# Kernel optimization log

Hardware: AMD Instinct MI355X
Metric: run time of the kernel (lower is better)

Reference implementation:

```python
import jax, jax.numpy as jnp
import numpy as np
import math

N = 512; B = 32; T_IN = 24; T_OUT = 12; C_IN = 1; C_OUT = 64
D_MODEL = 64; N_HEADS = 8; K = 3; N_LAYERS = 2; D_FF = 4 * D_MODEL
MA_KERNEL = 25; FACTOR = 1
E_HEAD = D_MODEL // N_HEADS


def _sin_pe(T, d):
    pos = jnp.arange(T, dtype=jnp.float32)[:, None]
    div = jnp.exp(jnp.arange(0, d, 2, dtype=jnp.float32) * (-math.log(10000.0) / d))
    pe = jnp.zeros((T, d), dtype=jnp.float32)
    pe = pe.at[:, 0::2].set(jnp.sin(pos * div))
    pe = pe.at[:, 1::2].set(jnp.cos(pos * div))
    return pe


def _moving_avg(x, k):
    # Autoformer series_decomp moving average with edge-replicate padding. x: (B,L,D)
    pad = (k - 1) // 2
    xp = jnp.concatenate([jnp.repeat(x[:, :1], pad, axis=1), x, jnp.repeat(x[:, -1:], pad, axis=1)], axis=1)
    cs = jnp.cumsum(xp, axis=1)
    cs = jnp.concatenate([jnp.zeros_like(cs[:, :1]), cs], axis=1)
    return (cs[:, k:] - cs[:, :-k]) / k


def _autocorr_attn(q, k, v):
    # Autoformer AutoCorrelation (eval-mode delay aggregation). q,k,v: (Bf,L,H,E)
    Bf, L, H, E = q.shape
    qf = jnp.fft.rfft(jnp.transpose(q, (0, 2, 3, 1)), axis=-1)
    kf = jnp.fft.rfft(jnp.transpose(k, (0, 2, 3, 1)), axis=-1)
    corr = jnp.fft.irfft(qf * jnp.conj(kf), n=L, axis=-1)      # (Bf,H,E,L)
    values = jnp.transpose(v, (0, 2, 3, 1))                    # (Bf,H,E,L)
    top_k = int(FACTOR * math.log(L))
    mean_value = corr.mean(axis=(1, 2))                        # (Bf,L)
    weights, delay = jax.lax.top_k(mean_value, top_k)          # (Bf,top_k)
    tmp_corr = jax.nn.softmax(weights, axis=-1)
    base = jnp.arange(L)[None, :]
    agg = jnp.zeros_like(values)
    for i in range(top_k):
        idx = (base + delay[:, i:i + 1]) % L                   # circular gather == repeat+gather
        pattern = jnp.take_along_axis(values, idx[:, None, None, :], axis=-1)
        agg = agg + pattern * tmp_corr[:, i][:, None, None, None]
    return jnp.transpose(agg, (0, 3, 1, 2))                    # (Bf,L,H,E)


def _forward(s_w, x, swnn_w, swnn_b, alpha, beta, theta, wq, bq, wk, bk, wv, bv, wo, bo,
             conv1_w, conv1_b, conv2_w, conv2_b, norm_g, norm_b, dec_w, dec_b,
             slin_w, slin_b, tlin_w, tlin_b):
    W = jax.nn.softmax(s_w @ swnn_w.T + swnn_b, axis=1)        # SWNN, n_hidden=1
    Lmat = jnp.diag(W.sum(axis=1)) - W
    lam = jax.lax.stop_gradient(jnp.max(jnp.real(jnp.linalg.eigvals(Lmat))))
    Lt = 2.0 * Lmat / lam - jnp.eye(N, dtype=x.dtype)
    chebs = [jnp.eye(N, dtype=x.dtype), Lt]
    for i in range(2, K):
        chebs.append(2.0 * Lt * chebs[-1] - chebs[-2])         # elementwise *, as in the source
    w_x = jnp.einsum('btnc,nm->btmc', x, W)
    s_acc = jnp.zeros((B, T_IN, N, C_OUT), dtype=x.dtype)
    for kk in range(K):
        s_r = alpha[kk] + jnp.einsum('btnc,co->btno', x, beta[kk]) + jnp.einsum('btnc,co->btno', w_x, theta[kk])
        s_acc = s_acc + jnp.einsum('btno,nm->btmo', s_r, chebs[kk])
    s_out = jax.nn.relu(jnp.transpose(s_acc, (0, 2, 3, 1)))    # (B,N,O,T_in)
    s_out = jnp.einsum('bnot,ut->bnou', s_out, slin_w) + slin_b  # (B,N,O,T_out)
    # ---- temporal branch: PE + AutoCorrelation encoder (AutoTRGCN) ----
    x_bnct = jnp.transpose(x, (0, 2, 3, 1))                    # (B,N,C,T)
    h = x_bnct[..., None] + _sin_pe(T_IN, D_MODEL)             # (B,N,C,T,D)
    h = h.reshape(B * N * C_IN, T_IN, D_MODEL)
    for _ in range(N_LAYERS):                                  # shared layer params, as in source
        q = (jnp.einsum('bld,ed->ble', h, wq) + bq).reshape(-1, T_IN, N_HEADS, E_HEAD)
        kt = (jnp.einsum('bld,ed->ble', h, wk) + bk).reshape(-1, T_IN, N_HEADS, E_HEAD)
        vt = (jnp.einsum('bld,ed->ble', h, wv) + bv).reshape(-1, T_IN, N_HEADS, E_HEAD)
        new_h = _autocorr_attn(q, kt, vt).reshape(-1, T_IN, D_MODEL)
        new_h = jnp.einsum('bld,ed->ble', new_h, wo) + bo
        h = h + new_h
        h = h - _moving_avg(h, MA_KERNEL)                      # series_decomp residual
        y = jax.nn.relu(jnp.einsum('bld,fd->blf', h, conv1_w) + conv1_b)
        y = jnp.einsum('blf,df->bld', y, conv2_w) + conv2_b
        hy = h + y
        h = hy - _moving_avg(hy, MA_KERNEL)
    mu = h.mean(-1, keepdims=True)
    var = ((h - mu) ** 2).mean(-1, keepdims=True)
    hn = (h - mu) / jnp.sqrt(var + 1e-5) * norm_g + norm_b
    h = hn - hn.mean(axis=1, keepdims=True)                    # my_Layernorm
    h = h.reshape(B, N, C_IN, T_IN * D_MODEL)
    t_out = jax.nn.relu(jnp.einsum('bnck,uk->bncu', h, dec_w) + dec_b)  # (B,N,C,T_out)
    t_out = jnp.einsum('bnct,oc->bnot', t_out, tlin_w) + tlin_b[None, None, :, None]  # (B,N,O,T_out)
    st = jax.nn.relu(s_out * t_out)
    return jnp.transpose(st, (0, 3, 1, 2))                     # (B,T_out,N,O)


def setup_inputs() -> dict:
    key = jax.random.key(0)
    ks = jax.random.split(key, 32)
    def rn(i, shape, scale=0.05):
        return jax.random.normal(ks[i], shape, dtype=jnp.float32) * scale
    return dict(
        s_w=jax.random.uniform(ks[0], (N, N), dtype=jnp.float32),
        x=jax.random.normal(ks[1], (B, T_IN, N, C_IN), dtype=jnp.float32),
        swnn_w=rn(2, (N, N)), swnn_b=rn(3, (N,)),
        alpha=rn(4, (K,)), beta=rn(5, (K, C_IN, C_OUT)), theta=rn(6, (K, C_IN, C_OUT)),
        wq=rn(7, (D_MODEL, D_MODEL)), bq=rn(8, (D_MODEL,)),
        wk=rn(9, (D_MODEL, D_MODEL)), bk=rn(10, (D_MODEL,)),
        wv=rn(11, (D_MODEL, D_MODEL)), bv=rn(12, (D_MODEL,)),
        wo=rn(13, (D_MODEL, D_MODEL)), bo=rn(14, (D_MODEL,)),
        conv1_w=rn(15, (D_FF, D_MODEL)), conv1_b=rn(16, (D_FF,)),
        conv2_w=rn(17, (D_MODEL, D_FF)), conv2_b=rn(18, (D_MODEL,)),
        norm_g=jnp.ones((D_MODEL,), dtype=jnp.float32), norm_b=jnp.zeros((D_MODEL,), dtype=jnp.float32),
        dec_w=rn(19, (T_OUT, D_MODEL * T_IN)), dec_b=rn(20, (T_OUT,)),
        slin_w=rn(21, (T_OUT, T_IN)), slin_b=rn(22, (T_OUT,)),
        tlin_w=rn(23, (C_OUT, C_IN)), tlin_b=rn(24, (C_OUT,)),
    )


def reference(s_w, x, swnn_w, swnn_b, alpha, beta, theta, wq, bq, wk, bk, wv, bv, wo, bo,
              conv1_w, conv1_b, conv2_w, conv2_b, norm_g, norm_b, dec_w, dec_b,
              slin_w, slin_b, tlin_w, tlin_b):
    return _forward(s_w, x, swnn_w, swnn_b, alpha, beta, theta, wq, bq, wk, bk, wv, bv, wo, bo,
                    conv1_w, conv1_b, conv2_w, conv2_b, norm_g, norm_b, dec_w, dec_b,
                    slin_w, slin_b, tlin_w, tlin_b)
```

## Files before the change

### kernel.cpp

```cpp
#include <hip/hip_runtime.h>
#include <hip/hip_bf16.h>
#include <math.h>


static const size_t OFF_W   = 0;
static const size_t OFF_SA  = OFF_W  + 512*512;
static const size_t OFF_SB  = OFF_SA + 512*512;
static const size_t OFF_WX  = OFF_SB + 512*512;
static const size_t OFF_Y1  = OFF_WX + 768*512;
static const size_t OFF_Y2  = OFF_Y1 + 768*512;
static const size_t OFF_Z1  = OFF_Y2 + 768*512;
static const size_t OFF_Z2  = OFF_Z1 + 768*512;
static const size_t OFF_TR  = OFF_Z2 + 768*512;
static const size_t OFF_PE  = OFF_TR + 16384*12;
static const size_t OFF_CS1 = OFF_PE + 24*64;
static const size_t OFF_CS2 = OFF_CS1 + 512;
static const size_t OFF_V0  = OFF_CS2 + 512;
static const size_t OFF_V1  = OFF_V0 + 512;
static const size_t OFF_NA  = OFF_V1 + 512;
static const size_t OFF_SC  = OFF_NA + 64;
static const size_t OFF_M   = OFF_SC + 16;
static const size_t OFF_PT  = OFF_M  + 4096;
static const size_t OFF_C1T = OFF_PT + 4096;
static const size_t OFF_C2T = OFF_C1T + 16384;
static const size_t OFF_BVO = OFF_C2T + 16384;

#define EIG_H 0.125f
#define EIG_K 14
#define MV_STEPS 32

__global__ __launch_bounds__(256) void k_prep(float* __restrict__ wsf) {
  const int t = threadIdx.x;
  for (int idx = t; idx < 24 * 64; idx += 256) {
    int l = idx >> 6, d = idx & 63;
    int i = d >> 1;
    float div = expf((float)(2 * i) * (-9.210340371976184f / 64.0f));
    float ang = (float)l * div;
    wsf[OFF_PE + idx] = (d & 1) ? cosf(ang) : sinf(ang);
  }
  for (int idx = t; idx < 512; idx += 256)
    wsf[OFF_V0 + idx] = sinf((float)idx * 12.9898f + 0.5f) + 0.01f;
  for (int idx = t; idx < 64; idx += 256)
    wsf[OFF_NA + idx] = 0.0f;
}

__global__ __launch_bounds__(256) void k_wprep(
    const float* __restrict__ wq, const float* __restrict__ wk,
    const float* __restrict__ wv, const float* __restrict__ wo,
    const float* __restrict__ bv, const float* __restrict__ bo,
    const float* __restrict__ c1w, const float* __restrict__ c2w,
    float* __restrict__ wsf) {
  const int blk = blockIdx.x, t = threadIdx.x;
  if (blk == 0) {
    for (int i = 0; i < 16; ++i) {
      int idx = i * 256 + t;
      int d = idx >> 6, dp = idx & 63;
      float s = 0.f;
      for (int e = 0; e < 64; ++e) s += wq[e * 64 + d] * wk[e * 64 + dp];
      wsf[OFF_M + idx] = s;
    }
    if (t < 64) {
      float s = bo[t];
      for (int f = 0; f < 64; ++f) s += wo[t * 64 + f] * bv[f];
      wsf[OFF_BVO + t] = s;
    }
  } else if (blk == 1) {
    for (int i = 0; i < 16; ++i) {
      int idx = i * 256 + t;
      int d = idx >> 6, e = idx & 63;
      float s = 0.f;
      for (int f = 0; f < 64; ++f) s += wo[e * 64 + f] * wv[f * 64 + d];
      wsf[OFF_PT + idx] = s;
    }
  } else if (blk < 4) {
    int base = (blk - 2) * 8192;
    for (int i = 0; i < 32; ++i) {
      int idx = base + i * 256 + t;
      int d = idx >> 8, f = idx & 255;
      wsf[OFF_C1T + idx] = c1w[f * 64 + d];
    }
  } else {
    int base = (blk - 4) * 8192;
    for (int i = 0; i < 32; ++i) {
      int idx = base + i * 256 + t;
      int f = idx >> 6, e = idx & 63;
      wsf[OFF_C2T + idx] = c2w[e * 256 + f];
    }
  }
}

__global__ __launch_bounds__(256) void k_gemm_logits(
    const float* __restrict__ A, const float* __restrict__ Bm,
    const float* __restrict__ bias, float* __restrict__ C) {
  __shared__ float As[32][33], Bs[32][33];
  const int tx = threadIdx.x & 31, ty = threadIdx.x >> 5;
  const int rb = blockIdx.y * 32, cb = blockIdx.x * 32;
  float acc[4] = {0.f, 0.f, 0.f, 0.f};
  for (int kk = 0; kk < 512; kk += 32) {
    for (int idx = threadIdx.x; idx < 1024; idx += 256) {
      int r = idx >> 5, c = idx & 31;
      As[r][c] = A[(rb + r) * 512 + kk + c];
      Bs[c][r] = Bm[(cb + r) * 512 + kk + c];
    }
    __syncthreads();
    for (int k2 = 0; k2 < 32; ++k2) {
      float bvv = Bs[k2][tx];
      #pragma unroll
      for (int i = 0; i < 4; ++i) acc[i] += As[ty + 8 * i][k2] * bvv;
    }
    __syncthreads();
  }
  float bb = bias[cb + tx];
  #pragma unroll
  for (int i = 0; i < 4; ++i)
    C[(rb + ty + 8 * i) * 512 + cb + tx] = acc[i] + bb;
}

__global__ __launch_bounds__(64) void k_softmax_rows(float* __restrict__ W) {
  const int r = blockIdx.x, t = threadIdx.x;
  float* row = W + (size_t)r * 512;
  float v[8];
  float mx = -3.4e38f;
  #pragma unroll
  for (int i = 0; i < 8; ++i) { v[i] = row[t + 64 * i]; mx = fmaxf(mx, v[i]); }
  for (int m = 1; m < 64; m <<= 1) mx = fmaxf(mx, __shfl_xor(mx, m));
  float s = 0.f;
  #pragma unroll
  for (int i = 0; i < 8; ++i) { v[i] = expf(v[i] - mx); s += v[i]; }
  for (int m = 1; m < 64; m <<= 1) s += __shfl_xor(s, m);
  float inv = 1.0f / s;
  #pragma unroll
  for (int i = 0; i < 8; ++i) row[t + 64 * i] = v[i] * inv;
}

__global__ __launch_bounds__(256) void k_init_S(float* __restrict__ wsf) {
  const int idx = blockIdx.x * 256 + threadIdx.x;
  const int i = idx >> 9, j = idx & 511;
  float w = wsf[OFF_W + idx];
  wsf[OFF_SA + idx] = ((i == j) ? 1.0f : 0.0f) - EIG_H * w;
  if (idx == 0) {
    wsf[OFF_SC + 0] = 0.0f;
    wsf[OFF_SC + 1] = 1.0f;
    ((unsigned int*)(wsf + OFF_SC))[8] = 0u;
  }
}

__global__ __launch_bounds__(256) void k_gemm_square(
    const float* __restrict__ A, float* __restrict__ C,
    const float* __restrict__ scal, unsigned int* __restrict__ mbits) {
  __shared__ float As[32][33], Bs[32][33];
  const int tx = threadIdx.x & 31, ty = threadIdx.x >> 5;
  const int rb = blockIdx.y * 32, cb = blockIdx.x * 32;
  float acc[4] = {0.f, 0.f, 0.f, 0.f};
  for (int kk = 0; kk < 512; kk += 32) {
    for (int idx = threadIdx.x; idx < 1024; idx += 256) {
      int r = idx >> 5, c = idx & 31;
      As[r][c] = A[(rb + r) * 512 + kk + c];
      Bs[r][c] = A[(kk + r) * 512 + cb + c];
    }
    __syncthreads();
    for (int k2 = 0; k2 < 32; ++k2) {
      float bvv = Bs[k2][tx];
      #pragma unroll
      for (int i = 0; i < 4; ++i) acc[i] += As[ty + 8 * i][k2] * bvv;
    }
    __syncthreads();
  }
  const float s = scal[1];
  const float s2 = s * s;
  float lmax = 0.f;
  #pragma unroll
  for (int i = 0; i < 4; ++i) {
    float v = acc[i] * s2;
    C[(rb + ty + 8 * i) * 512 + cb + tx] = v;
    lmax = fmaxf(lmax, fabsf(v));
  }
  for (int m = 1; m < 64; m <<= 1) lmax = fmaxf(lmax, __shfl_xor(lmax, m));
  if ((threadIdx.x & 63) == 0) atomicMax(mbits, __float_as_uint(lmax));
}

__global__ void k_bookkeep(float* __restrict__ wsf) {
  unsigned int* mb = (unsigned int*)(wsf + OFF_SC) + 8;
  float m = fmaxf(__uint_as_float(*mb), 1e-30f);
  wsf[OFF_SC + 0] = 2.0f * wsf[OFF_SC + 0] + logf(m);
  wsf[OFF_SC + 1] = 1.0f / m;
  *mb = 0u;
}

__global__ __launch_bounds__(64) void k_matvec(
    const float* __restrict__ S, const float* __restrict__ vin,
    float* __restrict__ vout, float* __restrict__ wsf, int p) {
  __shared__ float vv[512];
  const int t = threadIdx.x;
  const float invm = wsf[OFF_SC + 1];
  const float pn = (p == 0) ? 1.0f : fmaxf(wsf[OFF_NA + p - 1], 1e-30f);
  const float sc = invm / sqrtf(pn);
  for (int i = t; i < 512; i += 64) vv[i] = vin[i];
  __syncthreads();
  const int row = blockIdx.x * 64 + t;
  const float* rp = S + (size_t)row * 512;
  float acc = 0.f;
  for (int j = 0; j < 512; j += 4) {
    float4 a = *(const float4*)(rp + j);
    acc += a.x * vv[j] + a.y * vv[j + 1] + a.z * vv[j + 2] + a.w * vv[j + 3];
  }
  float y = acc * sc;
  vout[row] = y;
  float ss = y * y;
  for (int m = 1; m < 64; m <<= 1) ss += __shfl_xor(ss, m);
  if (t == 0) atomicAdd(&wsf[OFF_NA + p], ss);
}

__global__ void k_lamfin(float* __restrict__ wsf) {
  float slope = 0.f;
  for (int p = 8; p < 32; ++p) slope += 0.5f * logf(fmaxf(wsf[OFF_NA + p], 1e-30f));
  slope *= (1.0f / 24.0f);
  float rate = (slope + wsf[OFF_SC + 0]) * (1.0f / 16384.0f);
  float minre = (1.0f - expf(rate)) * (1.0f / EIG_H);
  float lam = 1.0f - minre;
  wsf[OFF_SC + 2] = lam;
  wsf[OFF_SC + 3] = 2.0f / lam - 1.0f;
  wsf[OFF_SC + 4] = 2.0f / lam;
}

__global__ __launch_bounds__(64) void k_colsum(const float* __restrict__ W,
                                               float* __restrict__ wsf) {
  const int m = blockIdx.x * 64 + threadIdx.x;
  float s1 = 0.f, s2 = 0.f;
  for (int n = 0; n < 512; ++n) {
    float w = W[n * 512 + m];
    s1 += w; s2 += w * w;
  }
  float wmm = W[m * 512 + m];
  float a = wsf[OFF_SC + 3], c = wsf[OFF_SC + 4];
  wsf[OFF_CS1 + m] = a - c * s1;
  wsf[OFF_CS2 + m] = 2.0f * (c * c * s2 + a * a - 2.0f * a * c * wmm) - 1.0f;
}

__global__ __launch_bounds__(256) void k_gemm_wx(
    const float* __restrict__ A, const float* __restrict__ Bm,
    float* __restrict__ C) {
  __shared__ float As[32][33], Bs[32][33];
  const int tx = threadIdx.x & 31, ty = threadIdx.x >> 5;
  const int rb = blockIdx.y * 32, cb = blockIdx.x * 32;
  float acc[4] = {0.f, 0.f, 0.f, 0.f};
  for (int kk = 0; kk < 512; kk += 32) {
    for (int idx = threadIdx.x; idx < 1024; idx += 256) {
      int r = idx >> 5, c = idx & 31;
      As[r][c] = A[(rb + r) * 512 + kk + c];
      Bs[r][c] = Bm[(kk + r) * 512 + cb + c];
    }
    __syncthreads();
    for (int k2 = 0; k2 < 32; ++k2) {
      float bvv = Bs[k2][tx];
      #pragma unroll
      for (int i = 0; i < 4; ++i) acc[i] += As[ty + 8 * i][k2] * bvv;
    }
    __syncthreads();
  }
  #pragma unroll
  for (int i = 0; i < 4; ++i)
    C[(rb + ty + 8 * i) * 512 + cb + tx] = acc[i];
}

__global__ __launch_bounds__(256) void k_gemm_yz(
    const float* __restrict__ X, const float* __restrict__ WX,
    const float* __restrict__ W, const float* __restrict__ sc,
    float* __restrict__ y1, float* __restrict__ y2,
    float* __restrict__ z1, float* __restrict__ z2) {
  __shared__ float Xs[32][33], Ms[32][33], C1s[32][33], C2s[32][33];
  const int tx = threadIdx.x & 31, ty = threadIdx.x >> 5;
  const int rb = blockIdx.y * 32, cb = blockIdx.x * 32;
  const float a = sc[3], c = sc[4];
  float ay1[4] = {0,0,0,0}, ay2[4] = {0,0,0,0}, az1[4] = {0,0,0,0}, az2[4] = {0,0,0,0};
  for (int kk = 0; kk < 512; kk += 32) {
    for (int idx = threadIdx.x; idx < 1024; idx += 256) {
      int r = idx >> 5, cc = idx & 31;
      Xs[r][cc] = X[(rb + r) * 512 + kk + cc];
      Ms[r][cc] = WX[(rb + r) * 512 + kk + cc];
      float w = W[(kk + r) * 512 + cb + cc];
      float dl = ((kk + r) == (cb + cc)) ? 1.0f : 0.0f;
      float c1 = a * dl - c * w;
      C1s[r][cc] = c1;
      C2s[r][cc] = 2.0f * c1 * c1 - dl;
    }
    __syncthreads();
    for (int k2 = 0; k2 < 32; ++k2) {
      float b1 = C1s[k2][tx], b2 = C2s[k2][tx];
      #pragma unroll
      for (int i = 0; i < 4; ++i) {
        float xv = Xs[ty + 8 * i][k2];
        float wv = Ms[ty + 8 * i][k2];
        ay1[i] += xv * b1; ay2[i] += xv * b2;
        az1[i] += wv * b1; az2[i] += wv * b2;
      }
    }
    __syncthreads();
  }
  #pragma unroll
  for (int i = 0; i < 4; ++i) {
    int off = (rb + ty + 8 * i) * 512 + cb + tx;
    y1[off] = ay1[i]; y2[off] = ay2[i];
    z1[off] = az1[i]; z2[off] = az2[i];
  }
}

#define HSTR 66
#define HSTR2 33

__device__ __forceinline__ void decomp_cols(float* __restrict__ hl, int t) {
  #pragma unroll
  for (int task = 0; task < 2; ++task) {
    int id = task * 256 + t;
    int sq = id >> 6, e = id & 63;
    int base = sq * 24 * HSTR + e;
    float h24[24];
    #pragma unroll
    for (int ll = 0; ll < 24; ++ll) h24[ll] = hl[base + ll * HSTR];
    float W = 13.0f * h24[0];
    #pragma unroll
    for (int j = 1; j <= 12; ++j) W += h24[j];
    #pragma unroll
    for (int ll = 0; ll < 24; ++ll) {
      hl[base + ll * HSTR] = h24[ll] - W * (1.0f / 25.0f);
      int jp = (ll + 13 > 23) ? 23 : ll + 13;
      int jm = (ll - 12 < 0) ? 0 : ll - 12;
      W += h24[jp] - h24[jm];
    }
  }
}

__global__ __launch_bounds__(256, 3) void k_temporal3(
    const float* __restrict__ x, const float* __restrict__ pe,
    const float* __restrict__ Mw, const float* __restrict__ PTw,
    const float* __restrict__ C1T, const float* __restrict__ C2T,
    const float* __restrict__ bvo,
    const float* __restrict__ c1b, const float* __restrict__ c2b,
    const float* __restrict__ ng, const float* __restrict__ nbv,
    const float* __restrict__ decw, const float* __restrict__ decb,
    float* __restrict__ trelu) {
  __shared__ float hl[8 * 24 * HSTR];
  __shared__ float aux[512];
  float* corr_s = aux;
  float* wsm_s  = aux + 192;
  int*   dly_s  = (int*)(aux + 216);
  float* cmean_s = aux;
  float* pr_s   = aux;

  const int t = threadIdx.x;
  const int s0 = blockIdx.x * 8;
  const bool active = t < 192;
  const int r = t;
  const int seq = r / 24;
  const int l = r - seq * 24;
  const int gseq = s0 + seq;
  const int b = gseq >> 9, n = gseq & 511;
  float2* hl2 = (float2*)hl;
  const int row2 = r * HSTR2;

  if (active) {
    float xv = x[(b * 24 + l) * 512 + n];
    const float2* per = (const float2*)(pe + l * 64);
    #pragma unroll
    for (int c = 0; c < 32; ++c) {
      float2 pv = per[c];
      hl2[row2 + c] = make_float2(xv + pv.x, xv + pv.y);
    }
  }
  __syncthreads();

  for (int layer = 0; layer < 2; ++layer) {
    if (t < 192) corr_s[t] = 0.f;
    __syncthreads();
    if (active) {
      float u[64];
      #pragma unroll
      for (int e = 0; e < 64; ++e) u[e] = 0.f;
      for (int dd = 0; dd < 32; ++dd) {
        float2 hv = hl2[row2 + dd];
        const float* M0 = Mw + (2 * dd) * 64;
        const float* M1 = M0 + 64;
        #pragma unroll
        for (int e = 0; e < 64; ++e) u[e] += hv.x * M0[e] + hv.y * M1[e];
      }
      for (int tau = 0; tau < 24; ++tau) {
        int l2v = l - tau; if (l2v < 0) l2v += 24;
        int bb2 = (seq * 24 + l2v) * HSTR2;
        float acc = 0.f;
        #pragma unroll
        for (int dd = 0; dd < 32; ++dd) {
          float2 h2 = hl2[bb2 + dd];
          acc += u[2 * dd] * h2.x + u[2 * dd + 1] * h2.y;
        }
        atomicAdd(&corr_s[seq * 24 + tau], acc * (1.0f / 64.0f));
      }
    }
    __syncthreads();
    if (t < 8) {
      const float* cr = corr_s + t * 24;
      int i0 = 0, i1 = 0, i2 = 0;
      float v0 = -3.4e38f, v1 = -3.4e38f, v2 = -3.4e38f;
      for (int j = 0; j < 24; ++j) { float v = cr[j]; if (v > v0) { v0 = v; i0 = j; } }
      for (int j = 0; j < 24; ++j) { if (j == i0) continue; float v = cr[j]; if (v > v1) { v1 = v; i1 = j; } }
      for (int j = 0; j < 24; ++j) { if (j == i0 || j == i1) continue; float v = cr[j]; if (v > v2) { v2 = v; i2 = j; } }
      float e1 = expf(v1 - v0), e2 = expf(v2 - v0);
      float inv = 1.0f / (1.0f + e1 + e2);
      wsm_s[t * 3] = inv; wsm_s[t * 3 + 1] = e1 * inv; wsm_s[t * 3 + 2] = e2 * inv;
      dly_s[t * 3] = i0; dly_s[t * 3 + 1] = i1; dly_s[t * 3 + 2] = i2;
    }
    __syncthreads();
    {
      float acc[64];
      #pragma unroll
      for (int e = 0; e < 64; ++e) acc[e] = 0.f;
      if (active) {
        float w0 = wsm_s[seq * 3], w1 = wsm_s[seq * 3 + 1], w2 = wsm_s[seq * 3 + 2];
        int d0 = dly_s[seq * 3], d1 = dly_s[seq * 3 + 1], d2 = dly_s[seq * 3 + 2];
        int l0 = l + d0; if (l0 >= 24) l0 -= 24;
        int l1 = l + d1; if (l1 >= 24) l1 -= 24;
        int l2 = l + d2; if (l2 >= 24) l2 -= 24;
        int b0 = (seq * 24 + l0) * HSTR2, b1 = (seq * 24 + l1) * HSTR2, b2 = (seq * 24 + l2) * HSTR2;
        for (int dd = 0; dd < 32; ++dd) {
          float2 a0 = hl2[b0 + dd], a1 = hl2[b1 + dd], av2 = hl2[b2 + dd];
          float gx = w0 * a0.x + w1 * a1.x + w2 * av2.x;
          float gy = w0 * a0.y + w1 * a1.y + w2 * av2.y;
          const float* P0 = PTw + (2 * dd) * 64;
          const float* P1 = P0 + 64;
          #pragma unroll
          for (int e = 0; e < 64; ++e) acc[e] += gx * P0[e] + gy * P1[e];
        }
      }
      __syncthreads();
      if (active) {
        #pragma unroll
        for (int j = 0; j < 32; ++j) {
          float2 cur = hl2[row2 + j];
          cur.x += acc[2 * j] + bvo[2 * j];
          cur.y += acc[2 * j + 1] + bvo[2 * j + 1];
          hl2[row2 + j] = cur;
        }
      }
    }
    __syncthreads();
    decomp_cols(hl, t);
    __syncthreads();
    {
      float a2[64];
      #pragma unroll
      for (int e = 0; e < 64; ++e) a2[e] = 0.f;
      if (active) {
        for (int fc = 0; fc < 16; ++fc) {
          float y16[16];
          #pragma unroll
          for (int f = 0; f < 16; ++f) y16[f] = 0.f;
          for (int dd = 0; dd < 32; ++dd) {
            float2 hv = hl2[row2 + dd];
            const float* c1a = C1T + (2 * dd) * 256 + fc * 16;
            const float* c1bp = c1a + 256;
            #pragma unroll
            for (int f = 0; f < 16; ++f) y16[f] += hv.x * c1a[f] + hv.y * c1bp[f];
          }
          #pragma unroll
          for (int f = 0; f < 16; ++f)
            y16[f] = fmaxf(y16[f] + c1b[fc * 16 + f], 0.0f);
          #pragma unroll
          for (int f = 0; f < 16; ++f) {
            float yf = y16[f];
            const float* r2 = C2T + (fc * 16 + f) * 64;
            #pragma unroll
            for (int e = 0; e < 64; ++e) a2[e] += yf * r2[e];
          }
        }
        #pragma unroll
        for (int j = 0; j < 32; ++j) {
          float2 cur = hl2[row2 + j];
          cur.x += a2[2 * j] + c2b[2 * j];
          cur.y += a2[2 * j + 1] + c2b[2 * j + 1];
          hl2[row2 + j] = cur;
        }
      }
    }
    __syncthreads();
    decomp_cols(hl, t);
    __syncthreads();
  }

  if (active) {
    float mu = 0.f;
    #pragma unroll
    for (int dd = 0; dd < 32; ++dd) { float2 v = hl2[row2 + dd]; mu += v.x + v.y; }
    mu *= (1.0f / 64.0f);
    float vs = 0.f;
    #pragma unroll
    for (int dd = 0; dd < 32; ++dd) {
      float2 v = hl2[row2 + dd];
      float dx = v.x - mu, dy = v.y - mu;
      vs += dx * dx + dy * dy;
    }
    float rs = rsqrtf(vs * (1.0f / 64.0f) + 1e-5f);
    #pragma unroll
    for (int dd = 0; dd < 32; ++dd) {
      float2 v = hl2[row2 + dd];
      v.x = (v.x - mu) * rs * ng[2 * dd] + nbv[2 * dd];
      v.y = (v.y - mu) * rs * ng[2 * dd + 1] + nbv[2 * dd + 1];
      hl2[row2 + dd] = v;
    }
  }
  __syncthreads();
  #pragma unroll
  for (int pass = 0; pass < 2; ++pass) {
    int idx = pass * 256 + t;
    int sq2 = idx >> 6, e2 = idx & 63;
    float s = 0.f;
    for (int ll = 0; ll < 24; ++ll) s += hl[(sq2 * 24 + ll) * HSTR + e2];
    cmean_s[idx] = s * (1.0f / 24.0f);
  }
  __syncthreads();
  if (active) {
    #pragma unroll
    for (int j = 0; j < 32; ++j) {
      float2 v = hl2[row2 + j];
      v.x -= cmean_s[seq * 64 + 2 * j];
      v.y -= cmean_s[seq * 64 + 2 * j + 1];
      hl2[row2 + j] = v;
    }
  }
  __syncthreads();
  if (active) {
    int g = t >> 3;
    int u = g >> 1, half = g & 1;
    int sq = t & 7;
    const float2* dwp2 = (const float2*)(decw + u * 1536 + half * 768);
    int hb2 = (sq * 24 + half * 12) * HSTR2;
    float part = 0.f;
    for (int j = 0; j < 384; ++j) {
      int lr = j >> 5, dd = j & 31;
      float2 hv = hl2[hb2 + lr * HSTR2 + dd];
      float2 wv = dwp2[j];
      part += hv.x * wv.x + hv.y * wv.y;
    }
    pr_s[t] = part;
  }
  __syncthreads();
  if (t < 96) {
    int u = t >> 3, sq = t & 7;
    float v = pr_s[(u * 2) * 8 + sq] + pr_s[(u * 2 + 1) * 8 + sq] + decb[u];
    trelu[(size_t)(s0 + sq) * 12 + u] = fmaxf(v, 0.0f);
  }
}

__global__ __launch_bounds__(64) void k_final(
    const float* __restrict__ x, const float* __restrict__ wx,
    const float* __restrict__ y1, const float* __restrict__ y2,
    const float* __restrict__ z1, const float* __restrict__ z2,
    const float* __restrict__ cs1, const float* __restrict__ cs2,
    const float* __restrict__ trelu,
    const float* __restrict__ alpha, const float* __restrict__ beta,
    const float* __restrict__ theta,
    const float* __restrict__ slinw, const float* __restrict__ slinb,
    const float* __restrict__ tlinw, const float* __restrict__ tlinb,
    float* __restrict__ out) {
  __shared__ float ly0[24], ly1[24], ly2[24], lz0[24], lz1[24], lz2[24];
  __shared__ float ltr[12], lsw[288];
  const int blk = blockIdx.x;
  const int b = blk >> 9, m = blk & 511;
  const int t = threadIdx.x;
  if (t < 24) {
    int row = (b * 24 + t) * 512 + m;
    ly0[t] = x[row];  ly1[t] = y1[row]; ly2[t] = y2[row];
    lz0[t] = wx[row]; lz1[t] = z1[row]; lz2[t] = z2[row];
  }
  if (t >= 48 && t < 60) ltr[t - 48] = trelu[(b * 512 + m) * 12 + (t - 48)];
  for (int i = t; i < 288; i += 64) lsw[i] = slinw[i];
  __syncthreads();
  const int o = t;
  const float at = alpha[0] + alpha[1] * cs1[m] + alpha[2] * cs2[m];
  const float b0 = beta[o], b1 = beta[64 + o], b2 = beta[128 + o];
  const float t0 = theta[o], t1 = theta[64 + o], t2 = theta[128 + o];
  float so[12];
  #pragma unroll
  for (int u = 0; u < 12; ++u) so[u] = 0.f;
  for (int tt = 0; tt < 24; ++tt) {
    float v = at + b0 * ly0[tt] + b1 * ly1[tt] + b2 * ly2[tt]
                 + t0 * lz0[tt] + t1 * lz1[tt] + t2 * lz2[tt];
    v = fmaxf(v, 0.0f);
    #pragma unroll
    for (int u = 0; u < 12; ++u) so[u] += lsw[u * 24 + tt] * v;
  }
  const float tw = tlinw[o], tb = tlinb[o];
  #pragma unroll
  for (int u = 0; u < 12; ++u) {
    float sval = so[u] + slinb[u];
    float tval = tw * ltr[u] + tb;
    float rr = fmaxf(sval * tval, 0.0f);
    out[(((size_t)b * 12 + u) * 512 + m) * 64 + o] = rr;
  }
}

extern "C" void kernel_launch(void* const* d_in, const int* in_sizes, int n_in,
                              void* d_out, int out_size, void* d_ws, size_t ws_size,
                              hipStream_t stream) {
  (void)in_sizes; (void)n_in; (void)out_size; (void)ws_size;
  const float* s_w    = (const float*)d_in[0];
  const float* x      = (const float*)d_in[1];
  const float* swnn_w = (const float*)d_in[2];
  const float* swnn_b = (const float*)d_in[3];
  const float* alpha  = (const float*)d_in[4];
  const float* beta   = (const float*)d_in[5];
  const float* theta  = (const float*)d_in[6];
  const float* wq = (const float*)d_in[7];  const float* bq = (const float*)d_in[8];
  const float* wk = (const float*)d_in[9];  const float* bk = (const float*)d_in[10];
  const float* wv = (const float*)d_in[11]; const float* bv = (const float*)d_in[12];
  const float* wo = (const float*)d_in[13]; const float* bo = (const float*)d_in[14];
  const float* c1w = (const float*)d_in[15]; const float* c1b = (const float*)d_in[16];
  const float* c2w = (const float*)d_in[17]; const float* c2b = (const float*)d_in[18];
  const float* ng  = (const float*)d_in[19]; const float* nb  = (const float*)d_in[20];
  const float* decw = (const float*)d_in[21]; const float* decb = (const float*)d_in[22];
  const float* slinw = (const float*)d_in[23]; const float* slinb = (const float*)d_in[24];
  const float* tlinw = (const float*)d_in[25]; const float* tlinb = (const float*)d_in[26];
  (void)bq; (void)bk;

  float* wsf = (float*)d_ws;
  float* out = (float*)d_out;

  float* Wm = wsf + OFF_W;
  float* Sa = wsf + OFF_SA;
  float* Sb = wsf + OFF_SB;
  unsigned int* mbits = (unsigned int*)(wsf + OFF_SC) + 8;
  const float* scal = wsf + OFF_SC;

  k_prep<<<1, 256, 0, stream>>>(wsf);
  k_wprep<<<6, 256, 0, stream>>>(wq, wk, wv, wo, bv, bo, c1w, c2w, wsf);
  k_gemm_logits<<<dim3(16, 16), 256, 0, stream>>>(s_w, swnn_w, swnn_b, Wm);
  k_softmax_rows<<<512, 64, 0, stream>>>(Wm);

  k_temporal3<<<2048, 256, 0, stream>>>(x, wsf + OFF_PE, wsf + OFF_M, wsf + OFF_PT,
                                        wsf + OFF_C1T, wsf + OFF_C2T, wsf + OFF_BVO,
                                        c1b, c2b, ng, nb, decw, decb, wsf + OFF_TR);

  k_init_S<<<1024, 256, 0, stream>>>(wsf);
  float* cur = Sa;
  float* nxt = Sb;
  for (int j = 0; j < EIG_K; ++j) {
    k_gemm_square<<<dim3(16, 16), 256, 0, stream>>>(cur, nxt, scal, mbits);
    k_bookkeep<<<1, 1, 0, stream>>>(wsf);
    float* tmp = cur; cur = nxt; nxt = tmp;
  }
  float* va = wsf + OFF_V0;
  float* vb = wsf + OFF_V1;
  for (int p = 0; p < MV_STEPS; ++p) {
    k_matvec<<<8, 64, 0, stream>>>(cur, va, vb, wsf, p);
    float* tmp = va; va = vb; vb = tmp;
  }
  k_lamfin<<<1, 1, 0, stream>>>(wsf);

  k_colsum<<<8, 64, 0, stream>>>(Wm, wsf);
  k_gemm_wx<<<dim3(16, 24), 256, 0, stream>>>(x, Wm, wsf + OFF_WX);
  k_gemm_yz<<<dim3(16, 24), 256, 0, stream>>>(x, wsf + OFF_WX, Wm, scal,
                                              wsf + OFF_Y1, wsf + OFF_Y2,
                                              wsf + OFF_Z1, wsf + OFF_Z2);
  k_final<<<16384, 64, 0, stream>>>(x, wsf + OFF_WX, wsf + OFF_Y1, wsf + OFF_Y2,
                                    wsf + OFF_Z1, wsf + OFF_Z2,
                                    wsf + OFF_CS1, wsf + OFF_CS2, wsf + OFF_TR,
                                    alpha, beta, theta, slinw, slinb,
                                    tlinw, tlinb, out);
}
```

Baseline: 2.888 ms.

## Enlarge square-GEMM tiles, halve power-iteration steps, vectorise temporal loads

The repeated-squaring GEMM moves from 32x32 tiles with 4 outputs per thread to 64x64 tiles with a 4x4 register micro-tile, so fewer blocks (64 instead of 256) each reuse shared-memory data more. The matvec power iteration drops from 32 to 16 steps, and the eigenvalue slope is now fit over steps 8-15 instead of 8-31, which may make the estimate less accurate. The temporal kernel's weight and bias reads are rewritten as float2 loads. The smaller GEMM grid leaves most of the device's compute units idle, trading parallelism for per-block efficiency.

```diff
diff --git a/kernel.cpp b/kernel.cpp
--- a/kernel.cpp
+++ b/kernel.cpp
@@ -27,7 +27,7 @@
 
 #define EIG_H 0.125f
 #define EIG_K 14
-#define MV_STEPS 32
+#define MV_STEPS 16
 
 __global__ __launch_bounds__(256) void k_prep(float* __restrict__ wsf) {
   const int t = threadIdx.x;
@@ -148,21 +148,32 @@
 __global__ __launch_bounds__(256) void k_gemm_square(
     const float* __restrict__ A, float* __restrict__ C,
     const float* __restrict__ scal, unsigned int* __restrict__ mbits) {
-  __shared__ float As[32][33], Bs[32][33];
-  const int tx = threadIdx.x & 31, ty = threadIdx.x >> 5;
-  const int rb = blockIdx.y * 32, cb = blockIdx.x * 32;
-  float acc[4] = {0.f, 0.f, 0.f, 0.f};
+  __shared__ float As[64][33], Bs[32][65];
+  const int t = threadIdx.x;
+  const int tr = t >> 4, tc = t & 15;
+  const int rb = blockIdx.y * 64, cb = blockIdx.x * 64;
+  float acc[4][4] = {{0.f}};
   for (int kk = 0; kk < 512; kk += 32) {
-    for (int idx = threadIdx.x; idx < 1024; idx += 256) {
+    #pragma unroll
+    for (int i = 0; i < 8; ++i) {
+      int idx = i * 256 + t;
       int r = idx >> 5, c = idx & 31;
       As[r][c] = A[(rb + r) * 512 + kk + c];
-      Bs[r][c] = A[(kk + r) * 512 + cb + c];
-    }
-    __syncthreads();
+      int r2 = idx >> 6, c2 = idx & 63;
+      Bs[r2][c2] = A[(kk + r2) * 512 + cb + c2];
+    }
+    __syncthreads();
+    #pragma unroll 8
     for (int k2 = 0; k2 < 32; ++k2) {
-      float bvv = Bs[k2][tx];
-      #pragma unroll
-      for (int i = 0; i < 4; ++i) acc[i] += As[ty + 8 * i][k2] * bvv;
+      float av[4], bw[4];
+      #pragma unroll
+      for (int i = 0; i < 4; ++i) av[i] = As[tr + 16 * i][k2];
+      #pragma unroll
+      for (int j = 0; j < 4; ++j) bw[j] = Bs[k2][tc + 16 * j];
+      #pragma unroll
+      for (int i = 0; i < 4; ++i)
+        #pragma unroll
+        for (int j = 0; j < 4; ++j) acc[i][j] += av[i] * bw[j];
     }
     __syncthreads();
   }
@@ -170,11 +181,13 @@
   const float s2 = s * s;
   float lmax = 0.f;
   #pragma unroll
-  for (int i = 0; i < 4; ++i) {
-    float v = acc[i] * s2;
-    C[(rb + ty + 8 * i) * 512 + cb + tx] = v;
-    lmax = fmaxf(lmax, fabsf(v));
-  }
+  for (int i = 0; i < 4; ++i)
+    #pragma unroll
+    for (int j = 0; j < 4; ++j) {
+      float v = acc[i][j] * s2;
+      C[(rb + tr + 16 * i) * 512 + cb + tc + 16 * j] = v;
+      lmax = fmaxf(lmax, fabsf(v));
+    }
   for (int m = 1; m < 64; m <<= 1) lmax = fmaxf(lmax, __shfl_xor(lmax, m));
   if ((threadIdx.x & 63) == 0) atomicMax(mbits, __float_as_uint(lmax));
 }
@@ -213,8 +226,8 @@
 
 __global__ void k_lamfin(float* __restrict__ wsf) {
   float slope = 0.f;
-  for (int p = 8; p < 32; ++p) slope += 0.5f * logf(fmaxf(wsf[OFF_NA + p], 1e-30f));
-  slope *= (1.0f / 24.0f);
+  for (int p = 8; p < 16; ++p) slope += 0.5f * logf(fmaxf(wsf[OFF_NA + p], 1e-30f));
+  slope *= (1.0f / 8.0f);
   float rate = (slope + wsf[OFF_SC + 0]) * (1.0f / 16384.0f);
   float minre = (1.0f - expf(rate)) * (1.0f / EIG_H);
   float lam = 1.0f - minre;
@@ -373,15 +386,19 @@
     if (t < 192) corr_s[t] = 0.f;
     __syncthreads();
     if (active) {
-      float u[64];
-      #pragma unroll
-      for (int e = 0; e < 64; ++e) u[e] = 0.f;
+      float2 u2[32];
+      #pragma unroll
+      for (int e = 0; e < 32; ++e) u2[e] = make_float2(0.f, 0.f);
       for (int dd = 0; dd < 32; ++dd) {
         float2 hv = hl2[row2 + dd];
-        const float* M0 = Mw + (2 * dd) * 64;
-        const float* M1 = M0 + 64;
+        const float2* M0 = (const float2*)(Mw + (2 * dd) * 64);
+        const float2* M1 = M0 + 32;
         #pragma unroll
-        for (int e = 0; e < 64; ++e) u[e] += hv.x * M0[e] + hv.y * M1[e];
+        for (int e = 0; e < 32; ++e) {
+          float2 m0 = M0[e], m1 = M1[e];
+          u2[e].x += hv.x * m0.x + hv.y * m1.x;
+          u2[e].y += hv.x * m0.y + hv.y * m1.y;
+        }
       }
       for (int tau = 0; tau < 24; ++tau) {
         int l2v = l - tau; if (l2v < 0) l2v += 24;
@@ -390,7 +407,7 @@
         #pragma unroll
         for (int dd = 0; dd < 32; ++dd) {
           float2 h2 = hl2[bb2 + dd];
-          acc += u[2 * dd] * h2.x + u[2 * dd + 1] * h2.y;
+          acc += u2[dd].x * h2.x + u2[dd].y * h2.y;
         }
         atomicAdd(&corr_s[seq * 24 + tau], acc * (1.0f / 64.0f));
       }
@@ -410,9 +427,9 @@
     }
     __syncthreads();
     {
-      float acc[64];
-      #pragma unroll
-      for (int e = 0; e < 64; ++e) acc[e] = 0.f;
+      float2 acc2[32];
+      #pragma unroll
+      for (int e = 0; e < 32; ++e) acc2[e] = make_float2(0.f, 0.f);
       if (active) {
         float w0 = wsm_s[seq * 3], w1 = wsm_s[seq * 3 + 1], w2 = wsm_s[seq * 3 + 2];
         int d0 = dly_s[seq * 3], d1 = dly_s[seq * 3 + 1], d2 = dly_s[seq * 3 + 2];
@@ -424,19 +441,25 @@
           float2 a0 = hl2[b0 + dd], a1 = hl2[b1 + dd], av2 = hl2[b2 + dd];
           float gx = w0 * a0.x + w1 * a1.x + w2 * av2.x;
           float gy = w0 * a0.y + w1 * a1.y + w2 * av2.y;
-          const float* P0 = PTw + (2 * dd) * 64;
-          const float* P1 = P0 + 64;
+          const float2* P0 = (const float2*)(PTw + (2 * dd) * 64);
+          const float2* P1 = P0 + 32;
           #pragma unroll
-          for (int e = 0; e < 64; ++e) acc[e] += gx * P0[e] + gy * P1[e];
+          for (int e = 0; e < 32; ++e) {
+            float2 p0 = P0[e], p1 = P1[e];
+            acc2[e].x += gx * p0.x + gy * p1.x;
+            acc2[e].y += gx * p0.y + gy * p1.y;
+          }
         }
       }
       __syncthreads();
       if (active) {
+        const float2* bvo2 = (const float2*)bvo;
         #pragma unroll
         for (int j = 0; j < 32; ++j) {
           float2 cur = hl2[row2 + j];
-          cur.x += acc[2 * j] + bvo[2 * j];
-          cur.y += acc[2 * j + 1] + bvo[2 * j + 1];
+          float2 bb = bvo2[j];
+          cur.x += acc2[j].x + bb.x;
+          cur.y += acc2[j].y + bb.y;
           hl2[row2 + j] = cur;
         }
       }
@@ -445,37 +468,51 @@
     decomp_cols(hl, t);
     __syncthreads();
     {
-      float a2[64];
-      #pragma unroll
-      for (int e = 0; e < 64; ++e) a2[e] = 0.f;
+      float2 a22[32];
+      #pragma unroll
+      for (int e = 0; e < 32; ++e) a22[e] = make_float2(0.f, 0.f);
       if (active) {
         for (int fc = 0; fc < 16; ++fc) {
-          float y16[16];
+          float2 y8[8];
           #pragma unroll
-          for (int f = 0; f < 16; ++f) y16[f] = 0.f;
+          for (int f = 0; f < 8; ++f) y8[f] = make_float2(0.f, 0.f);
           for (int dd = 0; dd < 32; ++dd) {
             float2 hv = hl2[row2 + dd];
-            const float* c1a = C1T + (2 * dd) * 256 + fc * 16;
-            const float* c1bp = c1a + 256;
+            const float2* c1a = (const float2*)(C1T + (2 * dd) * 256 + fc * 16);
+            const float2* c1bp = c1a + 128;
             #pragma unroll
-            for (int f = 0; f < 16; ++f) y16[f] += hv.x * c1a[f] + hv.y * c1bp[f];
+            for (int f = 0; f < 8; ++f) {
+              float2 wa = c1a[f], wb = c1bp[f];
+              y8[f].x += hv.x * wa.x + hv.y * wb.x;
+              y8[f].y += hv.x * wa.y + hv.y * wb.y;
+            }
+          }
+          const float2* c1b2 = (const float2*)(c1b + fc * 16);
+          #pragma unroll
+          for (int f = 0; f < 8; ++f) {
+            float2 bb = c1b2[f];
+            y8[f].x = fmaxf(y8[f].x + bb.x, 0.0f);
+            y8[f].y = fmaxf(y8[f].y + bb.y, 0.0f);
           }
           #pragma unroll
-          for (int f = 0; f < 16; ++f)
-            y16[f] = fmaxf(y16[f] + c1b[fc * 16 + f], 0.0f);
-          #pragma unroll
           for (int f = 0; f < 16; ++f) {
-            float yf = y16[f];
-            const float* r2 = C2T + (fc * 16 + f) * 64;
+            float yf = (f & 1) ? y8[f >> 1].y : y8[f >> 1].x;
+            const float2* r2 = (const float2*)(C2T + (fc * 16 + f) * 64);
             #pragma unroll
-            for (int e = 0; e < 64; ++e) a2[e] += yf * r2[e];
+            for (int e = 0; e < 32; ++e) {
+              float2 w2v = r2[e];
+              a22[e].x += yf * w2v.x;
+              a22[e].y += yf * w2v.y;
+            }
           }
         }
+        const float2* c2b2 = (const float2*)c2b;
         #pragma unroll
         for (int j = 0; j < 32; ++j) {
           float2 cur = hl2[row2 + j];
-          cur.x += a2[2 * j] + c2b[2 * j];
-          cur.y += a2[2 * j + 1] + c2b[2 * j + 1];
+          float2 bb = c2b2[j];
+          cur.x += a22[j].x + bb.x;
+          cur.y += a22[j].y + bb.y;
           hl2[row2 + j] = cur;
         }
       }
@@ -498,11 +535,14 @@
       vs += dx * dx + dy * dy;
     }
     float rs = rsqrtf(vs * (1.0f / 64.0f) + 1e-5f);
+    const float2* ng2 = (const float2*)ng;
+    const float2* nb2 = (const float2*)nbv;
     #pragma unroll
     for (int dd = 0; dd < 32; ++dd) {
       float2 v = hl2[row2 + dd];
-      v.x = (v.x - mu) * rs * ng[2 * dd] + nbv[2 * dd];
-      v.y = (v.y - mu) * rs * ng[2 * dd + 1] + nbv[2 * dd + 1];
+      float2 g = ng2[dd], bb = nb2[dd];
+      v.x = (v.x - mu) * rs * g.x + bb.x;
+      v.y = (v.y - mu) * rs * g.y + bb.y;
       hl2[row2 + dd] = v;
     }
   }
@@ -517,11 +557,12 @@
   }
   __syncthreads();
   if (active) {
+    const float2* cm2 = (const float2*)(cmean_s + seq * 64);
     #pragma unroll
     for (int j = 0; j < 32; ++j) {
       float2 v = hl2[row2 + j];
-      v.x -= cmean_s[seq * 64 + 2 * j];
-      v.y -= cmean_s[seq * 64 + 2 * j + 1];
+      float2 c = cm2[j];
+      v.x -= c.x; v.y -= c.y;
       hl2[row2 + j] = v;
     }
   }
@@ -642,7 +683,7 @@
   float* cur = Sa;
   float* nxt = Sb;
   for (int j = 0; j < EIG_K; ++j) {
-    k_gemm_square<<<dim3(16, 16), 256, 0, stream>>>(cur, nxt, scal, mbits);
+    k_gemm_square<<<dim3(8, 8), 256, 0, stream>>>(cur, nxt, scal, mbits);
     k_bookkeep<<<1, 1, 0, stream>>>(wsf);
     float* tmp = cur; cur = nxt; nxt = tmp;
   }
```

Result: slower. 3.257 ms (+12.8%).
